# Optimization experiments

Hardware: AMD Instinct MI355X
Metric: run time of the kernel (lower is better)

## Reference

```python
import jax, jax.numpy as jnp
import numpy as np
from jax import lax

MU = 0.1          # cfg MODEL.MU (FISTA step size)
LMBD = 0.1        # cfg MODEL.LAMBDA[0]
N_STEPS = 4       # cfg MODEL.NUM_LAYERS (unrolled FISTA iterations)
BN_EPS = 1e-5


def _norm_w(W):
    # DictBlock w_norm: each dictionary filter normalized to unit L2 norm.
    # torch does this under no_grad (in-place on .data), so the norm is a constant.
    n = jnp.sqrt(jnp.sum(W * W, axis=(1, 2, 3), keepdims=True))
    return W / lax.stop_gradient(n + 1e-12)


def _conv(x, W, stride, pad):
    return lax.conv_general_dilated(x, W, (stride, stride), [(pad, pad)] * 2,
                                    dimension_numbers=('NCHW', 'OIHW', 'NCHW'))


def _conv_t(z, W, stride, pad, out_pad):
    # torch conv_transpose2d(z, W, stride, padding=pad, output_padding=out_pad)
    k = W.shape[2]
    Wt = jnp.transpose(jnp.flip(W, (2, 3)), (1, 0, 2, 3))  # (in_ch, dict, k, k)
    p = k - 1 - pad
    return lax.conv_general_dilated(z, Wt, (1, 1), [(p, p + out_pad)] * 2,
                                    lhs_dilation=(stride, stride),
                                    dimension_numbers=('NCHW', 'OIHW', 'NCHW'))


def _shrink(c):
    # non-negative soft threshold: relu(c - lmbd*step)
    return jax.nn.relu(c - LMBD * MU)


def _dict_conv(x, W, stride):
    # Unrolled FISTA sparse coding: min_c 0.5||x - W^T c||^2 + lmbd||c||_1, c>=0
    W = _norm_w(W)
    out_pad = stride - 1
    c = _shrink(MU * _conv(x, W, stride, 1))
    c_pre = jnp.zeros_like(c)
    t = 1.0
    for _ in range(N_STEPS - 1):
        t_next = (1.0 + float(np.sqrt(1.0 + 4.0 * t * t))) / 2.0
        a = c + ((t - 1.0) / t_next) * (c - c_pre)
        c_pre = c
        r = x - _conv_t(a, W, stride, 1, out_pad)       # reconstruction residual
        c = _shrink(a + MU * _conv(r, W, stride, 1))    # proximal gradient step
        t = t_next
    return c


def _bn(x, g, b, m, v):
    # eval-mode BatchNorm2d with running stats
    scale = g * lax.rsqrt(v + BN_EPS)
    return (x - m[None, :, None, None]) * scale[None, :, None, None] + b[None, :, None, None]


def setup_inputs() -> dict:
    key = jax.random.key(0)
    ks = jax.random.split(key, 12)
    N, Cin, Cout, H = 32, 128, 256, 56
    x = jax.random.normal(ks[0], (N, Cin, H, H), jnp.float32)
    def unit_norm(W):
        return W / (jnp.sqrt(jnp.sum(W * W, axis=(1, 2, 3), keepdims=True)) + 1e-12)
    W1 = unit_norm(jax.random.normal(ks[1], (Cout, Cin, 3, 3), jnp.float32))
    W2 = unit_norm(jax.random.normal(ks[2], (Cout, Cout, 3, 3), jnp.float32))
    Wsc = jax.random.normal(ks[3], (Cout, Cin, 1, 1), jnp.float32) * 0.05
    def bn(k):
        k1, k2, k3, k4 = jax.random.split(k, 4)
        g = 1.0 + 0.1 * jax.random.normal(k1, (Cout,), jnp.float32)
        b = 0.1 * jax.random.normal(k2, (Cout,), jnp.float32)
        m = 0.1 * jax.random.normal(k3, (Cout,), jnp.float32)
        v = 0.5 + jax.random.uniform(k4, (Cout,), jnp.float32)
        return g, b, m, v
    bn1_g, bn1_b, bn1_m, bn1_v = bn(ks[4])
    bn2_g, bn2_b, bn2_m, bn2_v = bn(ks[5])
    bnsc_g, bnsc_b, bnsc_m, bnsc_v = bn(ks[6])
    return dict(x=x, W1=W1, W2=W2, Wsc=Wsc,
                bn1_g=bn1_g, bn1_b=bn1_b, bn1_m=bn1_m, bn1_v=bn1_v,
                bn2_g=bn2_g, bn2_b=bn2_b, bn2_m=bn2_m, bn2_v=bn2_v,
                bnsc_g=bnsc_g, bnsc_b=bnsc_b, bnsc_m=bnsc_m, bnsc_v=bnsc_v)


def reference(x, W1, W2, Wsc,
              bn1_g, bn1_b, bn1_m, bn1_v,
              bn2_g, bn2_b, bn2_m, bn2_v,
              bnsc_g, bnsc_b, bnsc_m, bnsc_v):
    out = _bn(_dict_conv(x, W1, 2), bn1_g, bn1_b, bn1_m, bn1_v)
    out = _bn(_dict_conv(out, W2, 1), bn2_g, bn2_b, bn2_m, bn2_v)
    sc = _bn(_conv(x, Wsc, 2, 0), bnsc_g, bnsc_b, bnsc_m, bnsc_v)
    return jax.nn.relu(out + sc)
```

## Files before the change

kernel.cpp:

```cpp
#include <hip/hip_runtime.h>
#include <math.h>

#define MU_F 0.1f
#define SHRINK_F 0.01f
#define BN_EPS_F 1e-5f

typedef _Float16 half_t;
typedef _Float16 half8 __attribute__((ext_vector_type(8)));
typedef _Float16 half4 __attribute__((ext_vector_type(4)));
typedef float f32x4 __attribute__((ext_vector_type(4)));

template<int KS, int S, int PAD, int MODE, int CAT>
__global__ __launch_bounds__(256, 1)
void conv_reg(const half_t* __restrict__ Af, const half_t* __restrict__ Xh,
              float* __restrict__ outF, half_t* __restrict__ outH,
              const half_t* __restrict__ auxH, const half_t* __restrict__ aux3H,
              const float* __restrict__ pscale, const float* __restrict__ pbias,
              int Cout, int Hin, int Win, int Hout, int Wout, int KT, int ptiles,
              float alpha, float beta, float delta, int relu1, int relu2)
{
    const int tid = threadIdx.x;
    const int wv = tid >> 6, ln = tid & 63;
    const int g  = blockIdx.y * 2 + (wv & 1);
    const int fr = ln & 15, rg = ln >> 4, ko8 = rg * 8;
    const int Hp = Hin + 2, Wp = Win + 2;

    int eh = 0, ew = 0, bx = blockIdx.x;
    if (MODE == 2) { int q = bx / ptiles; bx -= q * ptiles; eh = q >> 1; ew = q & 1; }
    const int p0 = bx * 128 + (wv >> 1) * 64;

    const int Wd   = (MODE == 2) ? (Wout >> 1) : Wout;
    const int Hd   = (MODE == 2) ? (Hout >> 1) : Hout;
    const int PHWI = Hd * Wd;

    int phv[4], pwv[4], nv[4], vb[4];
#pragma unroll
    for (int t = 0; t < 4; ++t) {
        int px = p0 + t * 16 + fr;
        int n  = px / PHWI; int rem = px - n * PHWI;
        int ph = rem / Wd;  int pw  = rem - ph * Wd;
        nv[t] = n; phv[t] = ph; pwv[t] = pw;
        int ih0 = (MODE == 0) ? ph * S : ph;
        int iw0 = (MODE == 0) ? pw * S : pw;
        vb[t] = ((n * Hp + ih0 + 1) * Wp + (iw0 + 1)) * CAT + ko8;
    }

    const half_t* Ap = Af + (size_t)g * KT * 2048 + ln * 8;
    constexpr int cpt = CAT / 32;
    constexpr int lgc = (cpt == 8) ? 3 : 2;
    int phh = 0, pww = 0, lgj = 0, ntap;
    if (MODE == 2) { phh = (eh + 1) & 1; pww = (ew + 1) & 1; lgj = ew; ntap = (1 + eh) * (1 + ew); }
    else           { ntap = KS * KS; }
    const int total = ntap << lgc;

    f32x4 acc[4][4] = {};

    auto fetch = [&](int k, half8 (&fa)[4], half8 (&fb)[4]) {
        const int ci = k & (cpt - 1), ti = k >> lgc;
        int kh, kw;
        if (MODE == 2) { int i2 = ti >> lgj, j = ti & ((1 << lgj) - 1); kh = phh + 2 * i2; kw = pww + 2 * j; }
        else           { kh = (ti * 11) >> 5; kw = ti - 3 * kh; }
        int dh, dw;
        if (MODE == 0)      { dh = kh - PAD;             dw = kw - PAD; }
        else if (MODE == 1) { dh = PAD - kh;             dw = PAD - kw; }
        else                { dh = (eh + PAD - kh) >> 1; dw = (ew + PAD - kw) >> 1; }
        const int off = (dh * Wp + dw) * CAT + (ci << 5);
#pragma unroll
        for (int t = 0; t < 4; ++t)
            fb[t] = *(const half8*)(Xh + (vb[t] + off));
        const int akc = (MODE == 2) ? ((kh * KS + kw) * cpt + ci) : k;
        const half_t* Apk = Ap + (size_t)akc * 2048;
#pragma unroll
        for (int m = 0; m < 4; ++m)
            fa[m] = *(const half8*)(Apk + m * 512);
    };
    auto mfma16 = [&](half8 (&fa)[4], half8 (&fb)[4]) {
#pragma unroll
        for (int m = 0; m < 4; ++m)
#pragma unroll
            for (int t = 0; t < 4; ++t)
                acc[m][t] = __builtin_amdgcn_mfma_f32_16x16x32_f16(fa[m], fb[t], acc[m][t], 0, 0, 0);
    };

    half8 SA0[4], SB0[4], SA1[4], SB1[4], SA2[4], SB2[4], SA3[4], SB3[4];
    fetch(0, SA0, SB0); fetch(1, SA1, SB1); fetch(2, SA2, SB2); fetch(3, SA3, SB3);
    for (int k = 0; k + 8 <= total; k += 4) {
        mfma16(SA0, SB0); fetch(k + 4, SA0, SB0);
        mfma16(SA1, SB1); fetch(k + 5, SA1, SB1);
        mfma16(SA2, SB2); fetch(k + 6, SA2, SB2);
        mfma16(SA3, SB3); fetch(k + 7, SA3, SB3);
    }
    mfma16(SA0, SB0); mfma16(SA1, SB1); mfma16(SA2, SB2); mfma16(SA3, SB3);

    const int Hpo = Hout + 2, Wpo = Wout + 2;
#pragma unroll
    for (int t = 0; t < 4; ++t) {
        int oh, ow;
        if (MODE == 2) { oh = 2 * phv[t] + eh; ow = 2 * pwv[t] + ew; }
        else           { oh = phv[t];          ow = pwv[t]; }
        size_t gb = ((size_t)(nv[t] * Hpo + oh + 1) * Wpo + (ow + 1)) * Cout + g * 64;
#pragma unroll
        for (int m = 0; m < 4; ++m) {
            const int cb = m * 16 + rg * 4;
            float v[4];
#pragma unroll
            for (int r = 0; r < 4; ++r) v[r] = alpha * acc[m][t][r] + delta;
            if (auxH) {
                half4 a1 = *(const half4*)(auxH + gb + cb);
#pragma unroll
                for (int r = 0; r < 4; ++r) v[r] += beta * (float)a1[r];
            }
            if (relu1)
#pragma unroll
                for (int r = 0; r < 4; ++r) v[r] = fmaxf(v[r], 0.f);
            if (pscale) {
                f32x4 s = *(const f32x4*)(pscale + g * 64 + cb);
                f32x4 b = *(const f32x4*)(pbias  + g * 64 + cb);
#pragma unroll
                for (int r = 0; r < 4; ++r) v[r] = s[r] * v[r] + b[r];
            }
            if (aux3H) {
                half4 a3 = *(const half4*)(aux3H + gb + cb);
#pragma unroll
                for (int r = 0; r < 4; ++r) v[r] += (float)a3[r];
            }
            if (relu2)
#pragma unroll
                for (int r = 0; r < 4; ++r) v[r] = fmaxf(v[r], 0.f);
            if (outH) {
                half4 o;
#pragma unroll
                for (int r = 0; r < 4; ++r) o[r] = (half_t)v[r];
                *(half4*)(outH + gb + cb) = o;
            } else {
                const int co = g * 64 + cb;
#pragma unroll
                for (int r = 0; r < 4; ++r)
                    outF[((size_t)(nv[t] * Cout + co + r) * Hout + oh) * Wout + ow] = v[r];
            }
        }
    }
}

template<int KT>
__global__ __launch_bounds__(256)
void pack_w(const float* __restrict__ W, half_t* __restrict__ Wh,
            half_t* __restrict__ WTh, int Cin, int Cout, int do_norm)
{
    __shared__ float red[256];
    int co = blockIdx.x, tid = threadIdx.x;
    int CK = Cin * KT;
    const float* w = W + (size_t)co * CK;
    float inv = 1.f;
    if (do_norm) {
        float s = 0.f;
        for (int i = tid; i < CK; i += 256) { float v = w[i]; s += v * v; }
        red[tid] = s; __syncthreads();
        for (int o = 128; o > 0; o >>= 1) {
            if (tid < o) red[tid] += red[tid + o];
            __syncthreads();
        }
        inv = 1.f / (sqrtf(red[0]) + 1e-12f);
    }
    for (int i = tid; i < CK; i += 256) {
        int ci = i / KT, tap = i - ci * KT;
        half_t h = (half_t)(w[i] * inv);
        Wh[((size_t)co * KT + tap) * Cin + ci] = h;
        if (WTh) WTh[((size_t)ci * KT + tap) * Cout + co] = h;
    }
}

__global__ __launch_bounds__(256)
void pack_frag(const half_t* __restrict__ Wflat, half_t* __restrict__ Af,
               int KT, int total8)
{
    int idx = blockIdx.x * 256 + threadIdx.x;
    if (idx >= total8) return;
    int l = idx & 63, m = (idx >> 6) & 3, t2 = idx >> 8;
    int kc = t2 % KT, gg = t2 / KT;
    int row = gg * 64 + m * 16 + (l & 15);
    int koff = kc * 32 + (l >> 4) * 8;
    int K9 = KT * 32;
    *(half8*)(Af + (size_t)idx * 8) = *(const half8*)(Wflat + (size_t)row * K9 + koff);
}

__global__ __launch_bounds__(256)
void tx_kernel(const float* __restrict__ x, half_t* __restrict__ xTh)
{
    __shared__ __align__(16) half_t tl[56 * 136];
    int h = blockIdx.x, n = blockIdx.y, tid = threadIdx.x;
    for (int it = 0; it < 28; ++it) {
        int id = tid + it * 256;
        int c = id / 56, w0 = id - c * 56;
        tl[w0 * 136 + c] = (half_t)x[(((size_t)n * 128 + c) * 56 + h) * 56 + w0];
    }
    __syncthreads();
    if (tid < 224) {
        int w0 = tid >> 2, part = tid & 3;
        size_t base = (((size_t)n * 58 + h + 1) * 58 + (w0 + 1)) * 128 + part * 32;
#pragma unroll
        for (int j = 0; j < 4; ++j)
            *(half8*)(xTh + base + j * 8) = *(const half8*)(tl + w0 * 136 + part * 32 + j * 8);
    }
}

__global__ __launch_bounds__(256)
void halo_zero(half_t* __restrict__ p, int Hp, int Wp, int C)
{
    int n = blockIdx.y;
    size_t base = (size_t)n * Hp * Wp * C;
    int per = 2 * Wp + 2 * (Hp - 2);
    int tot = per * C;
    for (int i = blockIdx.x * 256 + threadIdx.x; i < tot; i += gridDim.x * 256) {
        int pos = i / C, c = i - pos * C;
        int h, w;
        if (pos < Wp)            { h = 0;      w = pos; }
        else if (pos < 2 * Wp)   { h = Hp - 1; w = pos - Wp; }
        else { int r = pos - 2 * Wp; h = 1 + (r >> 1); w = (r & 1) ? (Wp - 1) : 0; }
        p[base + ((size_t)h * Wp + w) * C + c] = (half_t)0.f;
    }
}

__global__ __launch_bounds__(256)
void comb_kernel(const half_t* __restrict__ c, const half_t* __restrict__ p,
                 half_t* __restrict__ a, float w1, float w2, int n8)
{
    int i = blockIdx.x * 256 + threadIdx.x;
    if (i >= n8) return;
    half8 cv = ((const half8*)c)[i];
    half8 pv = ((const half8*)p)[i];
    half8 r;
#pragma unroll
    for (int j = 0; j < 8; ++j) r[j] = (half_t)(w1 * (float)cv[j] + w2 * (float)pv[j]);
    ((half8*)a)[i] = r;
}

__global__ __launch_bounds__(256)
void bn_prep_kernel(const float* __restrict__ g, const float* __restrict__ b,
                    const float* __restrict__ m, const float* __restrict__ v,
                    float* __restrict__ s, float* __restrict__ t, int C)
{
    int i = blockIdx.x * 256 + threadIdx.x;
    if (i < C) {
        float sc = g[i] * rsqrtf(v[i] + BN_EPS_F);
        s[i] = sc; t[i] = b[i] - m[i] * sc;
    }
}

extern "C" void kernel_launch(void* const* d_in, const int* in_sizes, int n_in,
                              void* d_out, int out_size, void* d_ws, size_t ws_size,
                              hipStream_t stream)
{
    (void)in_sizes; (void)n_in; (void)out_size;
    const float* x    = (const float*)d_in[0];
    const float* W1   = (const float*)d_in[1];
    const float* W2   = (const float*)d_in[2];
    const float* Wsc  = (const float*)d_in[3];
    const float* bn1g = (const float*)d_in[4];
    const float* bn1b = (const float*)d_in[5];
    const float* bn1m = (const float*)d_in[6];
    const float* bn1v = (const float*)d_in[7];
    const float* bn2g = (const float*)d_in[8];
    const float* bn2b = (const float*)d_in[9];
    const float* bn2m = (const float*)d_in[10];
    const float* bn2v = (const float*)d_in[11];
    const float* bscg = (const float*)d_in[12];
    const float* bscb = (const float*)d_in[13];
    const float* bscm = (const float*)d_in[14];
    const float* bscv = (const float*)d_in[15];

    const size_t P56 = (size_t)32 * 58 * 58 * 128;
    const size_t P28 = (size_t)32 * 30 * 30 * 256;

    char* base = (char*)d_ws;
    size_t off = 0;
    auto alloc = [&](size_t nbytes) -> void* {
        void* r = base + off;
        off = (off + nbytes + 255) & ~(size_t)255;
        return r;
    };
    half_t* Wh1  = (half_t*)alloc(294912 * 2);
    half_t* WTh1 = (half_t*)alloc(294912 * 2);
    half_t* Wh2  = (half_t*)alloc(589824 * 2);
    half_t* WTh2 = (half_t*)alloc(589824 * 2);
    half_t* Wsch = (half_t*)alloc(32768 * 2);
    half_t* Af1  = (half_t*)alloc(294912 * 2);
    half_t* AfT1 = (half_t*)alloc(294912 * 2);
    half_t* Af2  = (half_t*)alloc(589824 * 2);
    half_t* AfT2 = (half_t*)alloc(589824 * 2);
    half_t* Afsc = (half_t*)alloc(32768 * 2);
    float* bn1s = (float*)alloc(256 * 4);  float* bn1t = (float*)alloc(256 * 4);
    float* bn2s = (float*)alloc(256 * 4);  float* bn2t = (float*)alloc(256 * 4);
    float* bscs = (float*)alloc(256 * 4);  float* bsct = (float*)alloc(256 * 4);
    half_t* xTh  = (half_t*)alloc(P56 * 2);
    half_t* r56h = (half_t*)alloc(P56 * 2);
    half_t* Pa   = (half_t*)alloc(P28 * 2);
    half_t* Pb   = (half_t*)alloc(P28 * 2);
    half_t* Pc   = (half_t*)alloc(P28 * 2);
    half_t* Py   = (half_t*)alloc(P28 * 2);
    half_t* r28h = (half_t*)alloc(P28 * 2);
    half_t* Psc  = (half_t*)alloc(P28 * 2);
    if (off > ws_size) return;

    float* outp = (float*)d_out;

    double t = 1.0; float al[3];
    for (int i = 0; i < 3; ++i) {
        double tn = (1.0 + sqrt(1.0 + 4.0 * t * t)) / 2.0;
        al[i] = (float)((t - 1.0) / tn); t = tn;
    }

    const dim3 blk(256);
    const dim3 gF(196, 2);
    const dim3 gT2(784, 1);
    const int n8 = (int)(P28 / 8);
    const dim3 gC((n8 + 255) / 256);
    const float* NF = nullptr;
    const half_t* NH = nullptr;
    float* NFo = nullptr;
    half_t* NHo = nullptr;

    pack_w<9><<<256, blk, 0, stream>>>(W1, Wh1, WTh1, 128, 256, 1);
    pack_w<9><<<256, blk, 0, stream>>>(W2, Wh2, WTh2, 256, 256, 1);
    pack_w<1><<<256, blk, 0, stream>>>(Wsc, Wsch, nullptr, 128, 256, 0);
    pack_frag<<<(36864 + 255) / 256, blk, 0, stream>>>(Wh1,  Af1,  36, 36864);
    pack_frag<<<(36864 + 255) / 256, blk, 0, stream>>>(WTh1, AfT1, 72, 36864);
    pack_frag<<<(73728 + 255) / 256, blk, 0, stream>>>(Wh2,  Af2,  72, 73728);
    pack_frag<<<(73728 + 255) / 256, blk, 0, stream>>>(WTh2, AfT2, 72, 73728);
    pack_frag<<<(4096  + 255) / 256, blk, 0, stream>>>(Wsch, Afsc,  4, 4096);
    bn_prep_kernel<<<1, blk, 0, stream>>>(bn1g, bn1b, bn1m, bn1v, bn1s, bn1t, 256);
    bn_prep_kernel<<<1, blk, 0, stream>>>(bn2g, bn2b, bn2m, bn2v, bn2s, bn2t, 256);
    bn_prep_kernel<<<1, blk, 0, stream>>>(bscg, bscb, bscm, bscv, bscs, bsct, 256);
    halo_zero<<<dim3(8, 32), blk, 0, stream>>>(xTh,  58, 58, 128);
    halo_zero<<<dim3(8, 32), blk, 0, stream>>>(r56h, 58, 58, 128);
    halo_zero<<<dim3(8, 32), blk, 0, stream>>>(Pa,   30, 30, 256);
    halo_zero<<<dim3(8, 32), blk, 0, stream>>>(Pb,   30, 30, 256);
    halo_zero<<<dim3(8, 32), blk, 0, stream>>>(Pc,   30, 30, 256);
    halo_zero<<<dim3(8, 32), blk, 0, stream>>>(Py,   30, 30, 256);
    halo_zero<<<dim3(8, 32), blk, 0, stream>>>(r28h, 30, 30, 256);
    tx_kernel<<<dim3(56, 32), blk, 0, stream>>>(x, xTh);

    conv_reg<3,2,1,0,128><<<gF, blk, 0, stream>>>(Af1, xTh, NFo, Pa, NH, NH, NF, NF,
        256, 56, 56, 28, 28, 36, 196, MU_F, 0.f, -SHRINK_F, 1, 0);
    conv_reg<1,2,0,0,128><<<gF, blk, 0, stream>>>(Afsc, xTh, NFo, Psc, NH, NH, bscs, bsct,
        256, 56, 56, 28, 28, 4, 196, 1.f, 0.f, 0.f, 0, 0);

    conv_reg<3,2,1,2,256><<<gT2, blk, 0, stream>>>(AfT1, Pa, NFo, r56h, xTh, NH, NF, NF,
        128, 28, 28, 56, 56, 72, 196, -1.f, 1.f, 0.f, 0, 0);
    conv_reg<3,2,1,0,128><<<gF, blk, 0, stream>>>(Af1, r56h, NFo, Pb, Pa, NH, NF, NF,
        256, 56, 56, 28, 28, 36, 196, MU_F, 1.f, -SHRINK_F, 1, 0);

    comb_kernel<<<gC, blk, 0, stream>>>(Pb, Pa, Pc, 1.f + al[1], -al[1], n8);
    conv_reg<3,2,1,2,256><<<gT2, blk, 0, stream>>>(AfT1, Pc, NFo, r56h, xTh, NH, NF, NF,
        128, 28, 28, 56, 56, 72, 196, -1.f, 1.f, 0.f, 0, 0);
    conv_reg<3,2,1,0,128><<<gF, blk, 0, stream>>>(Af1, r56h, NFo, Pa, Pc, NH, NF, NF,
        256, 56, 56, 28, 28, 36, 196, MU_F, 1.f, -SHRINK_F, 1, 0);

    comb_kernel<<<gC, blk, 0, stream>>>(Pa, Pb, Pc, 1.f + al[2], -al[2], n8);
    conv_reg<3,2,1,2,256><<<gT2, blk, 0, stream>>>(AfT1, Pc, NFo, r56h, xTh, NH, NF, NF,
        128, 28, 28, 56, 56, 72, 196, -1.f, 1.f, 0.f, 0, 0);
    conv_reg<3,2,1,0,128><<<gF, blk, 0, stream>>>(Af1, r56h, NFo, Py, Pc, NH, bn1s, bn1t,
        256, 56, 56, 28, 28, 36, 196, MU_F, 1.f, -SHRINK_F, 1, 0);

    conv_reg<3,1,1,0,256><<<gF, blk, 0, stream>>>(Af2, Py, NFo, Pa, NH, NH, NF, NF,
        256, 28, 28, 28, 28, 72, 196, MU_F, 0.f, -SHRINK_F, 1, 0);

    conv_reg<3,1,1,1,256><<<gF, blk, 0, stream>>>(AfT2, Pa, NFo, r28h, Py, NH, NF, NF,
        256, 28, 28, 28, 28, 72, 196, -1.f, 1.f, 0.f, 0, 0);
    conv_reg<3,1,1,0,256><<<gF, blk, 0, stream>>>(Af2, r28h, NFo, Pb, Pa, NH, NF, NF,
        256, 28, 28, 28, 28, 72, 196, MU_F, 1.f, -SHRINK_F, 1, 0);

    comb_kernel<<<gC, blk, 0, stream>>>(Pb, Pa, Pc, 1.f + al[1], -al[1], n8);
    conv_reg<3,1,1,1,256><<<gF, blk, 0, stream>>>(AfT2, Pc, NFo, r28h, Py, NH, NF, NF,
        256, 28, 28, 28, 28, 72, 196, -1.f, 1.f, 0.f, 0, 0);
    conv_reg<3,1,1,0,256><<<gF, blk, 0, stream>>>(Af2, r28h, NFo, Pa, Pc, NH, NF, NF,
        256, 28, 28, 28, 28, 72, 196, MU_F, 1.f, -SHRINK_F, 1, 0);

    comb_kernel<<<gC, blk, 0, stream>>>(Pa, Pb, Pc, 1.f + al[2], -al[2], n8);
    conv_reg<3,1,1,1,256><<<gT2.x == 0 ? gF : gF, blk, 0, stream>>>(AfT2, Pc, NFo, r28h, Py, NH, NF, NF,
        256, 28, 28, 28, 28, 72, 196, -1.f, 1.f, 0.f, 0, 0);
    conv_reg<3,1,1,0,256><<<gF, blk, 0, stream>>>(Af2, r28h, outp, NHo, Pc, Psc, bn2s, bn2t,
        256, 28, 28, 28, 28, 72, 196, MU_F, 1.f, -SHRINK_F, 1, 1);
}
```

Measured before the change: 1.349 ms.

## Reorder K loop channel-major, halve prefetch depth, allow two blocks per CU

The conv kernel now walks the reduction channel-chunk-outer and tap-inner, and the weight fragments are repacked to match that order. The software prefetch ring drops from four stages to two, freeing registers so launch bounds can request two blocks per CU. The aim is higher occupancy to hide memory latency and better locality on activation reads across neighbouring taps. The cost is less in-flight prefetch per wave and possible spilling if the register budget is still too tight.

Measured after the change: 1.369 ms. Within noise of the previous version (+1.5%).

```diff
diff --git a/kernel.cpp b/kernel.cpp
--- a/kernel.cpp
+++ b/kernel.cpp
@@ -11,7 +11,7 @@
 typedef float f32x4 __attribute__((ext_vector_type(4)));
 
 template<int KS, int S, int PAD, int MODE, int CAT>
-__global__ __launch_bounds__(256, 1)
+__global__ __launch_bounds__(256, 2)
 void conv_reg(const half_t* __restrict__ Af, const half_t* __restrict__ Xh,
               float* __restrict__ outF, half_t* __restrict__ outH,
               const half_t* __restrict__ auxH, const half_t* __restrict__ aux3H,
@@ -24,6 +24,7 @@
     const int g  = blockIdx.y * 2 + (wv & 1);
     const int fr = ln & 15, rg = ln >> 4, ko8 = rg * 8;
     const int Hp = Hin + 2, Wp = Win + 2;
+    constexpr int ntapf = KS * KS;
 
     int eh = 0, ew = 0, bx = blockIdx.x;
     if (MODE == 2) { int q = bx / ptiles; bx -= q * ptiles; eh = q >> 1; ew = q & 1; }
@@ -47,19 +48,21 @@
 
     const half_t* Ap = Af + (size_t)g * KT * 2048 + ln * 8;
     constexpr int cpt = CAT / 32;
-    constexpr int lgc = (cpt == 8) ? 3 : 2;
-    int phh = 0, pww = 0, lgj = 0, ntap;
-    if (MODE == 2) { phh = (eh + 1) & 1; pww = (ew + 1) & 1; lgj = ew; ntap = (1 + eh) * (1 + ew); }
-    else           { ntap = KS * KS; }
-    const int total = ntap << lgc;
+    int phh = 0, pww = 0, lgj = 0, lgv = 0;
+    if (MODE == 2) { phh = (eh + 1) & 1; pww = (ew + 1) & 1; lgj = ew; lgv = eh + ew; }
+    const int ntapv = (MODE == 2) ? (1 << lgv) : ntapf;
+    const int total = cpt * ntapv;
 
     f32x4 acc[4][4] = {};
 
     auto fetch = [&](int k, half8 (&fa)[4], half8 (&fb)[4]) {
-        const int ci = k & (cpt - 1), ti = k >> lgc;
+        int ci, tv;
+        if (MODE == 2)      { ci = k >> lgv;       tv = k & (ntapv - 1); }
+        else if (KS == 3)   { ci = (k * 57) >> 9;  tv = k - ci * 9; }
+        else                { ci = k;              tv = 0; }
         int kh, kw;
-        if (MODE == 2) { int i2 = ti >> lgj, j = ti & ((1 << lgj) - 1); kh = phh + 2 * i2; kw = pww + 2 * j; }
-        else           { kh = (ti * 11) >> 5; kw = ti - 3 * kh; }
+        if (MODE == 2) { int i2 = tv >> lgj, j = tv & ((1 << lgj) - 1); kh = phh + 2 * i2; kw = pww + 2 * j; }
+        else           { kh = (tv * 11) >> 5; kw = tv - 3 * kh; }
         int dh, dw;
         if (MODE == 0)      { dh = kh - PAD;             dw = kw - PAD; }
         else if (MODE == 1) { dh = PAD - kh;             dw = PAD - kw; }
@@ -68,7 +71,7 @@
 #pragma unroll
         for (int t = 0; t < 4; ++t)
             fb[t] = *(const half8*)(Xh + (vb[t] + off));
-        const int akc = (MODE == 2) ? ((kh * KS + kw) * cpt + ci) : k;
+        const int akc = ci * ntapf + kh * KS + kw;
         const half_t* Apk = Ap + (size_t)akc * 2048;
 #pragma unroll
         for (int m = 0; m < 4; ++m)
@@ -82,15 +85,13 @@
                 acc[m][t] = __builtin_amdgcn_mfma_f32_16x16x32_f16(fa[m], fb[t], acc[m][t], 0, 0, 0);
     };
 
-    half8 SA0[4], SB0[4], SA1[4], SB1[4], SA2[4], SB2[4], SA3[4], SB3[4];
-    fetch(0, SA0, SB0); fetch(1, SA1, SB1); fetch(2, SA2, SB2); fetch(3, SA3, SB3);
-    for (int k = 0; k + 8 <= total; k += 4) {
-        mfma16(SA0, SB0); fetch(k + 4, SA0, SB0);
-        mfma16(SA1, SB1); fetch(k + 5, SA1, SB1);
-        mfma16(SA2, SB2); fetch(k + 6, SA2, SB2);
-        mfma16(SA3, SB3); fetch(k + 7, SA3, SB3);
-    }
-    mfma16(SA0, SB0); mfma16(SA1, SB1); mfma16(SA2, SB2); mfma16(SA3, SB3);
+    half8 SA0[4], SB0[4], SA1[4], SB1[4];
+    fetch(0, SA0, SB0); fetch(1, SA1, SB1);
+    for (int k = 0; k + 4 <= total; k += 2) {
+        mfma16(SA0, SB0); fetch(k + 2, SA0, SB0);
+        mfma16(SA1, SB1); fetch(k + 3, SA1, SB1);
+    }
+    mfma16(SA0, SB0); mfma16(SA1, SB1);
 
     const int Hpo = Hout + 2, Wpo = Wout + 2;
 #pragma unroll
@@ -172,14 +173,16 @@
 
 __global__ __launch_bounds__(256)
 void pack_frag(const half_t* __restrict__ Wflat, half_t* __restrict__ Af,
-               int KT, int total8)
+               int KT, int ntapf, int total8)
 {
     int idx = blockIdx.x * 256 + threadIdx.x;
     if (idx >= total8) return;
     int l = idx & 63, m = (idx >> 6) & 3, t2 = idx >> 8;
-    int kc = t2 % KT, gg = t2 / KT;
+    int f = t2 % KT, gg = t2 / KT;
+    int tap = f % ntapf, ci = f / ntapf;
+    int cpt = KT / ntapf;
     int row = gg * 64 + m * 16 + (l & 15);
-    int koff = kc * 32 + (l >> 4) * 8;
+    int koff = (tap * cpt + ci) * 32 + (l >> 4) * 8;
     int K9 = KT * 32;
     *(half8*)(Af + (size_t)idx * 8) = *(const half8*)(Wflat + (size_t)row * K9 + koff);
 }
@@ -323,11 +326,11 @@
     pack_w<9><<<256, blk, 0, stream>>>(W1, Wh1, WTh1, 128, 256, 1);
     pack_w<9><<<256, blk, 0, stream>>>(W2, Wh2, WTh2, 256, 256, 1);
     pack_w<1><<<256, blk, 0, stream>>>(Wsc, Wsch, nullptr, 128, 256, 0);
-    pack_frag<<<(36864 + 255) / 256, blk, 0, stream>>>(Wh1,  Af1,  36, 36864);
-    pack_frag<<<(36864 + 255) / 256, blk, 0, stream>>>(WTh1, AfT1, 72, 36864);
-    pack_frag<<<(73728 + 255) / 256, blk, 0, stream>>>(Wh2,  Af2,  72, 73728);
-    pack_frag<<<(73728 + 255) / 256, blk, 0, stream>>>(WTh2, AfT2, 72, 73728);
-    pack_frag<<<(4096  + 255) / 256, blk, 0, stream>>>(Wsch, Afsc,  4, 4096);
+    pack_frag<<<(36864 + 255) / 256, blk, 0, stream>>>(Wh1,  Af1,  36, 9, 36864);
+    pack_frag<<<(36864 + 255) / 256, blk, 0, stream>>>(WTh1, AfT1, 72, 9, 36864);
+    pack_frag<<<(73728 + 255) / 256, blk, 0, stream>>>(Wh2,  Af2,  72, 9, 73728);
+    pack_frag<<<(73728 + 255) / 256, blk, 0, stream>>>(WTh2, AfT2, 72, 9, 73728);
+    pack_frag<<<(4096  + 255) / 256, blk, 0, stream>>>(Wsch, Afsc,  4, 1, 4096);
     bn_prep_kernel<<<1, blk, 0, stream>>>(bn1g, bn1b, bn1m, bn1v, bn1s, bn1t, 256);
     bn_prep_kernel<<<1, blk, 0, stream>>>(bn2g, bn2b, bn2m, bn2v, bn2s, bn2t, 256);
     bn_prep_kernel<<<1, blk, 0, stream>>>(bscg, bscb, bscm, bscv, bscs, bsct, 256);
@@ -377,7 +380,7 @@
         256, 28, 28, 28, 28, 72, 196, MU_F, 1.f, -SHRINK_F, 1, 0);
 
     comb_kernel<<<gC, blk, 0, stream>>>(Pa, Pb, Pc, 1.f + al[2], -al[2], n8);
-    conv_reg<3,1,1,1,256><<<gT2.x == 0 ? gF : gF, blk, 0, stream>>>(AfT2, Pc, NFo, r28h, Py, NH, NF, NF,
+    conv_reg<3,1,1,1,256><<<gF, blk, 0, stream>>>(AfT2, Pc, NFo, r28h, Py, NH, NF, NF,
         256, 28, 28, 28, 28, 72, 196, -1.f, 1.f, 0.f, 0, 0);
     conv_reg<3,1,1,0,256><<<gF, blk, 0, stream>>>(Af2, r28h, outp, NHo, Pc, Psc, bn2s, bn2t,
         256, 28, 28, 28, 28, 72, 196, MU_F, 1.f, -SHRINK_F, 1, 1);
```
